# Performance work log

Hardware: AMD Instinct MI355X
Metric: run time of the kernel (lower is better)

The kernel has to match this reference:

```python
import jax, jax.numpy as jnp
import numpy as np
from jax import lax

DN = ('NCHW', 'OIHW', 'NCHW')

def _conv(x, k, stride):
    return lax.conv_general_dilated(x, k, (stride, stride), 'VALID', dimension_numbers=DN)

def setup_inputs() -> dict:
    key = jax.random.key(0)
    ks = jax.random.split(key, 20)
    B, E, A, D = 2048, 8, 6, 64 * 7 * 7  # batch, rm_states, actions, flat conv dim (3136)
    s = 0.05
    inp = {
        'state': jax.random.normal(ks[0], (B, 84, 84, 3), jnp.float32),
        'rm_state': jax.random.randint(ks[1], (B,), 0, E, jnp.int64),
        # conv encoder params
        'k1': jax.random.normal(ks[2], (32, 3, 8, 8), jnp.float32) * s,
        'c1': jnp.zeros((32,), jnp.float32),
        'k2': jax.random.normal(ks[3], (64, 32, 4, 4), jnp.float32) * s,
        'c2': jnp.zeros((64,), jnp.float32),
        'k3': jax.random.normal(ks[4], (64, 64, 3, 3), jnp.float32) * s,
        'c3': jnp.zeros((64,), jnp.float32),
        # stacked per-rm-state expert MLP params (E experts)
        'W1': jax.random.normal(ks[5], (E, D, 64), jnp.float32) * s,
        'B1': jnp.zeros((E, 64), jnp.float32),
        'W2': jax.random.normal(ks[6], (E, 64, 64), jnp.float32) * s,
        'B2': jnp.zeros((E, 64), jnp.float32),
        'W3': jax.random.normal(ks[7], (E, 64, 64), jnp.float32) * s,
        'B3': jnp.zeros((E, 64), jnp.float32),
        'W4': jax.random.normal(ks[8], (E, 64, 64), jnp.float32) * s,
        'B4': jnp.zeros((E, 64), jnp.float32),
        'W5': jax.random.normal(ks[9], (E, 64, 64), jnp.float32) * s,
        'B5': jnp.zeros((E, 64), jnp.float32),
        'W6': jax.random.normal(ks[10], (E, 64, A), jnp.float32) * s,
        'B6': jnp.zeros((E, A), jnp.float32),
    }
    return inp

def reference(state, rm_state, k1, c1, k2, c2, k3, c3,
              W1, B1, W2, B2, W3, B3, W4, B4, W5, B5, W6, B6):
    # NHWC -> NCHW (matches torch's view-based channel-first rearrangement intent)
    x = jnp.transpose(state, (0, 3, 1, 2))
    x = jax.nn.relu(_conv(x, k1, 4) + c1[None, :, None, None])
    x = jax.nn.relu(_conv(x, k2, 2) + c2[None, :, None, None])
    x = jax.nn.relu(_conv(x, k3, 1) + c3[None, :, None, None])
    B = x.shape[0]
    flat = x.reshape(B, -1)                              # [B, 3136]
    # batched expert MLPs: compute all experts, then gather per-sample expert output
    h = jax.nn.relu(jnp.einsum('bd,edh->ebh', flat, W1) + B1[:, None, :])  # [E,B,64]
    for W, Bb in ((W2, B2), (W3, B3), (W4, B4), (W5, B5)):
        h = jax.nn.relu(jnp.einsum('ebh,ehk->ebk', h, W) + Bb[:, None, :])
    out = jnp.einsum('ebh,eha->eba', h, W6) + B6[:, None, :]               # [E,B,A]
    return out[rm_state, jnp.arange(B)]                  # [B, A]
```

## Files before the change

kernel.cpp:

```cpp
#include <hip/hip_runtime.h>

#define BATCH 2048

typedef unsigned short u16;
typedef __attribute__((ext_vector_type(8))) short bf16x8;
typedef __attribute__((ext_vector_type(4))) float f32x4;

static __device__ __forceinline__ float b2f(u16 h) {
  union { unsigned u; float f; } x; x.u = ((unsigned)h) << 16; return x.f;
}
static __device__ __forceinline__ u16 f2b(float f) {
  union { float f; unsigned u; } x; x.f = f;
  return (u16)((x.u + 0x7fffu + ((x.u >> 16) & 1u)) >> 16);
}
static __device__ __forceinline__ void split2(float v, u16& h, u16& l) {
  h = f2b(v); l = f2b(v - b2f(h));
}
static __device__ __forceinline__ bf16x8 ld8u(const u16* p, int idx) {
  union { bf16x8 v; ushort4 u[2]; } x;
  x.u[0] = *(const ushort4*)(p + idx);
  x.u[1] = *(const ushort4*)(p + idx + 4);
  return x.v;
}

__global__ void wsplit_kernel(const float* __restrict__ k1,
                              const float* __restrict__ k2,
                              const float* __restrict__ k3,
                              u16* __restrict__ W1d, u16* __restrict__ W2d,
                              u16* __restrict__ W3d)
{
  int id = blockIdx.x * 256 + threadIdx.x;
  float v; u16 *dh, *dl;
  if (id < 8192) {
    int ky = id >> 10, oc = (id >> 5) & 31, kk = id & 31;
    if (kk < 24) {
      int kx = kk / 3, c = kk - kx * 3;
      v = k1[oc * 192 + c * 64 + ky * 8 + kx];
    } else v = 0.f;
    dh = W1d + id; dl = W1d + 8192 + id;
  } else if (id < 40960) {
    int i = id - 8192;
    int pos = i >> 11, oc = (i >> 5) & 63, cc = i & 31;
    int ky = pos >> 2, kx = pos & 3;
    v = k2[oc * 512 + cc * 16 + ky * 4 + kx];
    dh = W2d + i; dl = W2d + 32768 + i;
  } else {
    int i = id - 40960;
    int j = i & 31, oc = (i >> 5) & 63, kc = (i >> 11) & 1, pos = i >> 12;
    int ky = pos / 3, kx = pos - ky * 3;
    v = k3[oc * 576 + (kc * 32 + j) * 9 + ky * 3 + kx];
    dh = W3d + i; dl = W3d + 36864 + i;
  }
  u16 h, l; split2(v, h, l); *dh = h; *dl = l;
}

__global__ __launch_bounds__(256) void conv_fused_kernel(
    const float* __restrict__ state, const u16* __restrict__ W1d,
    const u16* __restrict__ W2d, const u16* __restrict__ W3d,
    const float* __restrict__ c1, const float* __restrict__ c2,
    const float* __restrict__ c3, float* __restrict__ a3)
{
  __shared__ __align__(16) u16 A1h[14400], A1l[14400];
  __shared__ __align__(16) u16 SHa[5832], SHb[5832];

  const int b = blockIdx.x, t = threadIdx.x;
  const int lane = t & 63, w = t >> 6, q = lane >> 4, n = lane & 15;

  for (int i = t; i < 792; i += 256) { SHa[5040 + i] = 0; SHb[5040 + i] = 0; }

  const bool two = (w < 2);
  const int nPT = two ? 2 : 1, nOT = two ? 2 : 1;
  int ptv[2], otv[2];
  ptv[0] = two ? 2 * w     : 4;
  ptv[1] = two ? 2 * w + 1 : 4;
  otv[0] = two ? 0 : (w - 2);
  otv[1] = 1;

  int aoff1[2];
  #pragma unroll
  for (int i = 0; i < 2; ++i) {
    int px = ptv[i] * 16 + n; if (px > 79) px = 79;
    int py = (px * 205) >> 12, pxx = px - py * 20;
    aoff1[i] = (py * 4) * 252 + pxx * 12 + q * 8;
  }
  float c1v[2];
  #pragma unroll
  for (int j = 0; j < 2; ++j) c1v[j] = c1[otv[j] * 16 + n];

  for (int by = 0; by < 5; ++by) {
    __syncthreads();
    const float4* sp = (const float4*)(state + (size_t)b * 21168 + by * 4032);
    #pragma unroll
    for (int pass = 0; pass < 5; ++pass) {
      int i = t + pass * 256;
      if (i < 1260) {
        float4 v = sp[i];
        u16 h0, l0, h1, l1, h2, l2, h3, l3;
        split2(v.x, h0, l0); split2(v.y, h1, l1);
        split2(v.z, h2, l2); split2(v.w, h3, l3);
        ushort4 hh; hh.x = h0; hh.y = h1; hh.z = h2; hh.w = h3;
        ushort4 ll; ll.x = l0; ll.y = l1; ll.z = l2; ll.w = l3;
        *(ushort4*)&SHa[i * 4] = hh;
        *(ushort4*)&SHb[i * 4] = ll;
      }
    }
    __syncthreads();

    f32x4 acc[2][2] = {};
    for (int ky = 0; ky < 8; ++ky) {
      bf16x8 bh[2], bo[2];
      #pragma unroll
      for (int j = 0; j < 2; ++j) if (j < nOT) {
        int ob = (ky * 32 + otv[j] * 16 + n) * 32 + q * 8;
        bh[j] = *(const bf16x8*)(W1d + ob);
        bo[j] = *(const bf16x8*)(W1d + 8192 + ob);
      }
      #pragma unroll
      for (int i = 0; i < 2; ++i) if (i < nPT) {
        bf16x8 ah = ld8u(SHa, aoff1[i] + ky * 252);
        bf16x8 al = ld8u(SHb, aoff1[i] + ky * 252);
        #pragma unroll
        for (int j = 0; j < 2; ++j) if (j < nOT) {
          acc[i][j] = __builtin_amdgcn_mfma_f32_16x16x32_bf16(ah, bh[j], acc[i][j], 0, 0, 0);
          acc[i][j] = __builtin_amdgcn_mfma_f32_16x16x32_bf16(ah, bo[j], acc[i][j], 0, 0, 0);
          acc[i][j] = __builtin_amdgcn_mfma_f32_16x16x32_bf16(al, bh[j], acc[i][j], 0, 0, 0);
        }
      }
    }
    #pragma unroll
    for (int i = 0; i < 2; ++i) if (i < nPT)
      #pragma unroll
      for (int j = 0; j < 2; ++j) if (j < nOT) {
        int oc = otv[j] * 16 + n;
        #pragma unroll
        for (int r = 0; r < 4; ++r) {
          int px = by * 80 + ptv[i] * 16 + q * 4 + r;
          float v = fmaxf(acc[i][j][r] + c1v[j], 0.f);
          u16 h, l; split2(v, h, l);
          A1h[px * 36 + oc] = h; A1l[px * 36 + oc] = l;
        }
      }
  }
  __syncthreads();

  {
    const int p20 = (w >> 1) * 3, o20 = (w & 1) * 2;
    int aoff2[3];
    #pragma unroll
    for (int i = 0; i < 3; ++i) {
      int px = (p20 + i) * 16 + n; if (px > 80) px = 80;
      int py = (px * 7282) >> 16, pxx = px - py * 9;
      aoff2[i] = 2 * (py * 20 + pxx) * 36 + q * 8;
    }
    float c2v[2];
    #pragma unroll
    for (int j = 0; j < 2; ++j) c2v[j] = c2[(o20 + j) * 16 + n];

    f32x4 acc2[3][2] = {};
    for (int pos = 0; pos < 16; ++pos) {
      const int o = ((pos >> 2) * 20 + (pos & 3)) * 36;
      bf16x8 bh[2], bo[2];
      #pragma unroll
      for (int j = 0; j < 2; ++j) {
        int ob = pos * 2048 + ((o20 + j) * 16 + n) * 32 + q * 8;
        bh[j] = *(const bf16x8*)(W2d + ob);
        bo[j] = *(const bf16x8*)(W2d + 32768 + ob);
      }
      #pragma unroll
      for (int i = 0; i < 3; ++i) {
        bf16x8 ah = ld8u(A1h, aoff2[i] + o);
        bf16x8 al = ld8u(A1l, aoff2[i] + o);
        #pragma unroll
        for (int j = 0; j < 2; ++j) {
          acc2[i][j] = __builtin_amdgcn_mfma_f32_16x16x32_bf16(ah, bh[j], acc2[i][j], 0, 0, 0);
          acc2[i][j] = __builtin_amdgcn_mfma_f32_16x16x32_bf16(ah, bo[j], acc2[i][j], 0, 0, 0);
          acc2[i][j] = __builtin_amdgcn_mfma_f32_16x16x32_bf16(al, bh[j], acc2[i][j], 0, 0, 0);
        }
      }
    }
    #pragma unroll
    for (int i = 0; i < 3; ++i)
      #pragma unroll
      for (int j = 0; j < 2; ++j) {
        int oc = (o20 + j) * 16 + n;
        #pragma unroll
        for (int r = 0; r < 4; ++r) {
          int px = (p20 + i) * 16 + q * 4 + r;
          if (px < 81) {
            float v = fmaxf(acc2[i][j][r] + c2v[j], 0.f);
            u16 h, l; split2(v, h, l);
            SHa[px * 72 + oc] = h; SHb[px * 72 + oc] = l;
          }
        }
      }
  }
  __syncthreads();

  {
    const int p30 = (w >> 1) * 2, o30 = (w & 1) * 2;
    int aoff3[2];
    #pragma unroll
    for (int i = 0; i < 2; ++i) {
      int px = (p30 + i) * 16 + n; if (px > 48) px = 48;
      int py = (px * 74) >> 9, pxx = px - py * 7;
      aoff3[i] = (py * 9 + pxx) * 72 + q * 8;
    }
    float c3v[2];
    #pragma unroll
    for (int j = 0; j < 2; ++j) c3v[j] = c3[(o30 + j) * 16 + n];

    f32x4 acc3[2][2] = {};
    for (int pos = 0; pos < 9; ++pos) {
      int ky = pos / 3, kx = pos - ky * 3;
      const int o = (ky * 9 + kx) * 72;
      #pragma unroll
      for (int kc = 0; kc < 2; ++kc) {
        bf16x8 bh[2], bo[2];
        #pragma unroll
        for (int j = 0; j < 2; ++j) {
          int ob = (pos * 2 + kc) * 2048 + ((o30 + j) * 16 + n) * 32 + q * 8;
          bh[j] = *(const bf16x8*)(W3d + ob);
          bo[j] = *(const bf16x8*)(W3d + 36864 + ob);
        }
        #pragma unroll
        for (int i = 0; i < 2; ++i) {
          bf16x8 ah = *(const bf16x8*)&SHa[aoff3[i] + o + kc * 32];
          bf16x8 al = *(const bf16x8*)&SHb[aoff3[i] + o + kc * 32];
          #pragma unroll
          for (int j = 0; j < 2; ++j) {
            acc3[i][j] = __builtin_amdgcn_mfma_f32_16x16x32_bf16(ah, bh[j], acc3[i][j], 0, 0, 0);
            acc3[i][j] = __builtin_amdgcn_mfma_f32_16x16x32_bf16(ah, bo[j], acc3[i][j], 0, 0, 0);
            acc3[i][j] = __builtin_amdgcn_mfma_f32_16x16x32_bf16(al, bh[j], acc3[i][j], 0, 0, 0);
          }
        }
      }
    }
    float* op = a3 + (size_t)b * 3136;
    #pragma unroll
    for (int i = 0; i < 2; ++i)
      #pragma unroll
      for (int j = 0; j < 2; ++j) {
        int oc = (o30 + j) * 16 + n;
        #pragma unroll
        for (int r = 0; r < 4; ++r) {
          int px = (p30 + i) * 16 + q * 4 + r;
          if (px < 49) op[oc * 49 + px] = fmaxf(acc3[i][j][r] + c3v[j], 0.f);
        }
      }
  }
}

__global__ void group_kernel(const void* __restrict__ rmv,
                             int* __restrict__ counts, int* __restrict__ idxb)
{
  __shared__ int isI32;
  const int t = threadIdx.x;
  if (t == 0) isI32 = 0;
  if (t < 8) counts[t] = 0;
  __syncthreads();
  unsigned long long v = ((const unsigned long long*)rmv)[t];
  if (v >= 8ull) isI32 = 1;
  __syncthreads();
  const int i32 = isI32;
  for (int b = t; b < BATCH; b += 1024) {
    int e = i32 ? ((const int*)rmv)[b] : (int)((const long long*)rmv)[b];
    int pos = atomicAdd(&counts[e], 1);
    idxb[e * BATCH + pos] = b;
  }
}

__global__ __launch_bounds__(256) void gemm1_grp_kernel(
    const float* __restrict__ a3, const int* __restrict__ counts,
    const int* __restrict__ idxb, const float* __restrict__ W1,
    float* __restrict__ H1)
{
  __shared__ __align__(16) float At[32 * 68];
  __shared__ __align__(16) float Bw[32 * 64];
  __shared__ int s_id[64];
  const int e  = blockIdx.x >> 5;
  const int tl = blockIdx.x & 31;
  const int ks = blockIdx.y;
  const int cnt = counts[e];
  const int n0 = tl * 64;
  if (n0 >= cnt) return;
  const int m = min(64, cnt - n0);
  const int t = threadIdx.x;
  if (t < 64) s_id[t] = idxb[e * BATCH + n0 + min(t, m - 1)];
  __syncthreads();

  const int tx = t & 15, ty = t >> 4;
  const int c0 = tx * 4, r0 = ty * 4;
  const float* W1e = W1 + (size_t)e * 3136 * 64;
  float acc[4][4] = {};
  const int kbase = ks * 448;

  for (int k0 = kbase; k0 < kbase + 448; k0 += 32) {
    __syncthreads();
    {
      int i = t;
      #pragma unroll
      for (int pass = 0; pass < 2; ++pass, i += 256) {
        int r = i >> 3, k4 = (i & 7) * 4;
        float4 v = *(const float4*)(a3 + (size_t)s_id[r] * 3136 + k0 + k4);
        At[(k4 + 0) * 68 + r] = v.x; At[(k4 + 1) * 68 + r] = v.y;
        At[(k4 + 2) * 68 + r] = v.z; At[(k4 + 3) * 68 + r] = v.w;
      }
      int i2 = t;
      #pragma unroll
      for (int pass = 0; pass < 2; ++pass, i2 += 256) {
        int kk = i2 >> 4, h4 = (i2 & 15) * 4;
        *(float4*)&Bw[kk * 64 + h4] = *(const float4*)&W1e[(size_t)(k0 + kk) * 64 + h4];
      }
    }
    __syncthreads();
    #pragma unroll
    for (int kk = 0; kk < 32; ++kk) {
      float4 a = *(const float4*)&At[kk * 68 + r0];
      float4 bb = *(const float4*)&Bw[kk * 64 + c0];
      float av[4] = {a.x, a.y, a.z, a.w}, bv[4] = {bb.x, bb.y, bb.z, bb.w};
      #pragma unroll
      for (int ii = 0; ii < 4; ++ii)
        #pragma unroll
        for (int j = 0; j < 4; ++j)
          acc[ii][j] += av[ii] * bv[j];
    }
  }

  #pragma unroll
  for (int ii = 0; ii < 4; ++ii) {
    if (r0 + ii < m) {
      int s = s_id[r0 + ii];
      #pragma unroll
      for (int j = 0; j < 4; ++j)
        atomicAdd(&H1[(size_t)s * 64 + c0 + j], acc[ii][j]);
    }
  }
}

__global__ __launch_bounds__(256) void tail_grp_kernel(
    const float* __restrict__ H1, const int* __restrict__ counts,
    const int* __restrict__ idxb, const float* __restrict__ B1,
    const float* __restrict__ W2, const float* __restrict__ B2,
    const float* __restrict__ W3, const float* __restrict__ B3,
    const float* __restrict__ W4, const float* __restrict__ B4,
    const float* __restrict__ W5, const float* __restrict__ B5,
    const float* __restrict__ W6, const float* __restrict__ B6,
    float* __restrict__ out)
{
  __shared__ __align__(16) float Wl[4096];
  __shared__ float bl[64];
  __shared__ float W6l[384];
  __shared__ float B6l[8];
  __shared__ __align__(16) float Ht0[64 * 68];
  __shared__ __align__(16) float Ht1[64 * 68];
  __shared__ int s_id[64];

  const int e  = blockIdx.x >> 5;
  const int tl = blockIdx.x & 31;
  const int cnt = counts[e];
  const int n0 = tl * 64;
  if (n0 >= cnt) return;
  const int m = min(64, cnt - n0);
  const int t = threadIdx.x;
  if (t < 64) s_id[t] = idxb[e * BATCH + n0 + min(t, m - 1)];
  for (int i = t; i < 384; i += 256) W6l[i] = W6[e * 384 + i];
  if (t < 6)   B6l[t] = B6[e * 6 + t];
  __syncthreads();

  #pragma unroll
  for (int p = 0; p < 16; ++p) {
    int i = t + p * 256;
    int c = i & 63, r = i >> 6;
    Ht0[c * 68 + r] = fmaxf(H1[(size_t)s_id[r] * 64 + c] + B1[e * 64 + c], 0.f);
  }

  const int tx = t & 15, ty = t >> 4;
  const int c0 = tx * 4, r0 = ty * 4;
  const float* Ws[4] = {W2, W3, W4, W5};
  const float* Bs[4] = {B2, B3, B4, B5};
  float* Hc = Ht0; float* Hn = Ht1;

  for (int L = 0; L < 4; ++L) {
    __syncthreads();
    const float* We = Ws[L] + (size_t)e * 4096;
    for (int i = t; i < 1024; i += 256)
      *(float4*)&Wl[i * 4] = *(const float4*)&We[i * 4];
    if (t < 64) bl[t] = Bs[L][e * 64 + t];
    __syncthreads();

    float acc[4][4] = {};
    #pragma unroll 4
    for (int kk = 0; kk < 64; ++kk) {
      float4 a = *(const float4*)&Hc[kk * 68 + r0];
      float4 bb = *(const float4*)&Wl[kk * 64 + c0];
      float av[4] = {a.x, a.y, a.z, a.w}, bv[4] = {bb.x, bb.y, bb.z, bb.w};
      #pragma unroll
      for (int ii = 0; ii < 4; ++ii)
        #pragma unroll
        for (int j = 0; j < 4; ++j)
          acc[ii][j] += av[ii] * bv[j];
    }
    __syncthreads();
    #pragma unroll
    for (int j = 0; j < 4; ++j) {
      float bias = bl[c0 + j];
      #pragma unroll
      for (int ii = 0; ii < 4; ++ii)
        Hn[(c0 + j) * 68 + r0 + ii] = fmaxf(acc[ii][j] + bias, 0.f);
    }
    float* tmp = Hc; Hc = Hn; Hn = tmp;
  }
  __syncthreads();

  const int r = t & 63, aa = t >> 6;
  float s0v = 0.f, s1v = 0.f;
  for (int k = 0; k < 64; ++k) {
    float h = Hc[k * 68 + r];
    s0v += h * W6l[k * 6 + aa];
    s1v += h * W6l[k * 6 + ((aa < 2) ? aa + 4 : aa)];
  }
  if (r < m) {
    int s = s_id[r];
    out[s * 6 + aa] = s0v + B6l[aa];
    if (aa < 2) out[s * 6 + aa + 4] = s1v + B6l[aa + 4];
  }
}

extern "C" void kernel_launch(void* const* d_in, const int* in_sizes, int n_in,
                              void* d_out, int out_size, void* d_ws, size_t ws_size,
                              hipStream_t stream) {
  const float* state = (const float*)d_in[0];
  const void*  rm    = d_in[1];
  const float* k1 = (const float*)d_in[2];
  const float* c1 = (const float*)d_in[3];
  const float* k2 = (const float*)d_in[4];
  const float* c2 = (const float*)d_in[5];
  const float* k3 = (const float*)d_in[6];
  const float* c3 = (const float*)d_in[7];
  const float* W1 = (const float*)d_in[8];
  const float* B1 = (const float*)d_in[9];
  const float* W2 = (const float*)d_in[10];
  const float* B2 = (const float*)d_in[11];
  const float* W3 = (const float*)d_in[12];
  const float* B3 = (const float*)d_in[13];
  const float* W4 = (const float*)d_in[14];
  const float* B4 = (const float*)d_in[15];
  const float* W5 = (const float*)d_in[16];
  const float* B5 = (const float*)d_in[17];
  const float* W6 = (const float*)d_in[18];
  const float* B6 = (const float*)d_in[19];

  char* ws = (char*)d_ws;
  float* a3   = (float*)(ws);
  float* H1   = (float*)(ws + 25690112);
  int* counts = (int*)  (ws + 26214400);
  int* idxb   = (int*)  (ws + 26214432);
  u16* W1d    = (u16*)  (ws + 26280064);
  u16* W2d    = (u16*)  (ws + 26312832);
  u16* W3d    = (u16*)  (ws + 26443904);

  wsplit_kernel<<<304, 256, 0, stream>>>(k1, k2, k3, W1d, W2d, W3d);
  hipMemsetAsync(H1, 0, BATCH * 64 * sizeof(float), stream);
  group_kernel<<<1, 1024, 0, stream>>>(rm, counts, idxb);

  conv_fused_kernel<<<2048, 256, 0, stream>>>(state, W1d, W2d, W3d,
                                              c1, c2, c3, a3);

  gemm1_grp_kernel<<<dim3(256, 7), 256, 0, stream>>>(a3, counts, idxb, W1, H1);
  tail_grp_kernel<<<256, 256, 0, stream>>>(H1, counts, idxb, B1,
                                           W2, B2, W3, B3, W4, B4, W5, B5,
                                           W6, B6, (float*)d_out);
}
```

Before: 539.8 us.

## Use 512-thread blocks in fused conv and prefetch weight fragments

Each conv block now has 8 waves instead of 4. Every wave owns a single output-channel tile and fewer pixel tiles in all three conv stages, and the state load uses 3 passes instead of 5. Weight fragments for the next kernel position are loaded one step ahead, a register double buffer meant to hide global load latency behind the MFMAs. Launch bounds change to (512,4) to request higher occupancy, which could cap registers and cause spills. Shared memory per block stays about the same.

```diff
diff --git a/kernel.cpp b/kernel.cpp
--- a/kernel.cpp
+++ b/kernel.cpp
@@ -54,7 +54,7 @@
   u16 h, l; split2(v, h, l); *dh = h; *dl = l;
 }
 
-__global__ __launch_bounds__(256) void conv_fused_kernel(
+__global__ __launch_bounds__(512, 4) void conv_fused_kernel(
     const float* __restrict__ state, const u16* __restrict__ W1d,
     const u16* __restrict__ W2d, const u16* __restrict__ W3d,
     const float* __restrict__ c1, const float* __restrict__ c2,
@@ -66,33 +66,32 @@
   const int b = blockIdx.x, t = threadIdx.x;
   const int lane = t & 63, w = t >> 6, q = lane >> 4, n = lane & 15;
 
-  for (int i = t; i < 792; i += 256) { SHa[5040 + i] = 0; SHb[5040 + i] = 0; }
-
-  const bool two = (w < 2);
-  const int nPT = two ? 2 : 1, nOT = two ? 2 : 1;
-  int ptv[2], otv[2];
-  ptv[0] = two ? 2 * w     : 4;
-  ptv[1] = two ? 2 * w + 1 : 4;
-  otv[0] = two ? 0 : (w - 2);
-  otv[1] = 1;
+  for (int i = t; i < 792; i += 512) { SHa[5040 + i] = 0; SHb[5040 + i] = 0; }
+
+  const int nT1 = (w < 2) ? 2 : 1;
+  int pt1[2], ot1[2];
+  if (w < 2) { pt1[0] = 0; ot1[0] = w; pt1[1] = 4; ot1[1] = w; }
+  else       { pt1[0] = 1 + ((w - 2) >> 1); ot1[0] = (w - 2) & 1;
+               pt1[1] = pt1[0]; ot1[1] = ot1[0]; }
 
   int aoff1[2];
   #pragma unroll
   for (int i = 0; i < 2; ++i) {
-    int px = ptv[i] * 16 + n; if (px > 79) px = 79;
+    int px = pt1[i] * 16 + n;
     int py = (px * 205) >> 12, pxx = px - py * 20;
     aoff1[i] = (py * 4) * 252 + pxx * 12 + q * 8;
   }
   float c1v[2];
   #pragma unroll
-  for (int j = 0; j < 2; ++j) c1v[j] = c1[otv[j] * 16 + n];
+  for (int j = 0; j < 2; ++j) c1v[j] = c1[ot1[j] * 16 + n];
+  const int ob1 = (ot1[0] * 16 + n) * 32 + q * 8;
 
   for (int by = 0; by < 5; ++by) {
     __syncthreads();
     const float4* sp = (const float4*)(state + (size_t)b * 21168 + by * 4032);
     #pragma unroll
-    for (int pass = 0; pass < 5; ++pass) {
-      int i = t + pass * 256;
+    for (int pass = 0; pass < 3; ++pass) {
+      int i = t + pass * 512;
       if (i < 1260) {
         float4 v = sp[i];
         u16 h0, l0, h1, l1, h2, l2, h3, l3;
@@ -106,147 +105,125 @@
     }
     __syncthreads();
 
-    f32x4 acc[2][2] = {};
+    f32x4 acc1[2] = {};
+    bf16x8 bhc = *(const bf16x8*)(W1d + ob1);
+    bf16x8 boc = *(const bf16x8*)(W1d + 8192 + ob1);
     for (int ky = 0; ky < 8; ++ky) {
-      bf16x8 bh[2], bo[2];
-      #pragma unroll
-      for (int j = 0; j < 2; ++j) if (j < nOT) {
-        int ob = (ky * 32 + otv[j] * 16 + n) * 32 + q * 8;
-        bh[j] = *(const bf16x8*)(W1d + ob);
-        bo[j] = *(const bf16x8*)(W1d + 8192 + ob);
-      }
-      #pragma unroll
-      for (int i = 0; i < 2; ++i) if (i < nPT) {
+      const int kyn = (ky < 7) ? ky + 1 : 7;
+      bf16x8 bhn = *(const bf16x8*)(W1d + kyn * 1024 + ob1);
+      bf16x8 bon = *(const bf16x8*)(W1d + 8192 + kyn * 1024 + ob1);
+      #pragma unroll
+      for (int i = 0; i < 2; ++i) if (i < nT1) {
         bf16x8 ah = ld8u(SHa, aoff1[i] + ky * 252);
         bf16x8 al = ld8u(SHb, aoff1[i] + ky * 252);
-        #pragma unroll
-        for (int j = 0; j < 2; ++j) if (j < nOT) {
-          acc[i][j] = __builtin_amdgcn_mfma_f32_16x16x32_bf16(ah, bh[j], acc[i][j], 0, 0, 0);
-          acc[i][j] = __builtin_amdgcn_mfma_f32_16x16x32_bf16(ah, bo[j], acc[i][j], 0, 0, 0);
-          acc[i][j] = __builtin_amdgcn_mfma_f32_16x16x32_bf16(al, bh[j], acc[i][j], 0, 0, 0);
-        }
-      }
-    }
-    #pragma unroll
-    for (int i = 0; i < 2; ++i) if (i < nPT)
-      #pragma unroll
-      for (int j = 0; j < 2; ++j) if (j < nOT) {
-        int oc = otv[j] * 16 + n;
-        #pragma unroll
-        for (int r = 0; r < 4; ++r) {
-          int px = by * 80 + ptv[i] * 16 + q * 4 + r;
-          float v = fmaxf(acc[i][j][r] + c1v[j], 0.f);
-          u16 h, l; split2(v, h, l);
-          A1h[px * 36 + oc] = h; A1l[px * 36 + oc] = l;
-        }
-      }
+        acc1[i] = __builtin_amdgcn_mfma_f32_16x16x32_bf16(ah, bhc, acc1[i], 0, 0, 0);
+        acc1[i] = __builtin_amdgcn_mfma_f32_16x16x32_bf16(ah, boc, acc1[i], 0, 0, 0);
+        acc1[i] = __builtin_amdgcn_mfma_f32_16x16x32_bf16(al, bhc, acc1[i], 0, 0, 0);
+      }
+      bhc = bhn; boc = bon;
+    }
+    #pragma unroll
+    for (int i = 0; i < 2; ++i) if (i < nT1) {
+      int oc = ot1[i] * 16 + n;
+      #pragma unroll
+      for (int r = 0; r < 4; ++r) {
+        int px = by * 80 + pt1[i] * 16 + q * 4 + r;
+        float v = fmaxf(acc1[i][r] + c1v[i], 0.f);
+        u16 h, l; split2(v, h, l);
+        A1h[px * 36 + oc] = h; A1l[px * 36 + oc] = l;
+      }
+    }
   }
   __syncthreads();
 
   {
-    const int p20 = (w >> 1) * 3, o20 = (w & 1) * 2;
+    const int ot2 = w & 3, pg2 = (w >> 2) * 3;
     int aoff2[3];
     #pragma unroll
     for (int i = 0; i < 3; ++i) {
-      int px = (p20 + i) * 16 + n; if (px > 80) px = 80;
+      int px = (pg2 + i) * 16 + n; if (px > 80) px = 80;
       int py = (px * 7282) >> 16, pxx = px - py * 9;
       aoff2[i] = 2 * (py * 20 + pxx) * 36 + q * 8;
     }
-    float c2v[2];
-    #pragma unroll
-    for (int j = 0; j < 2; ++j) c2v[j] = c2[(o20 + j) * 16 + n];
-
-    f32x4 acc2[3][2] = {};
+    const float c2v = c2[ot2 * 16 + n];
+    const int ob2 = (ot2 * 16 + n) * 32 + q * 8;
+
+    f32x4 acc2[3] = {};
+    bf16x8 bhc = *(const bf16x8*)(W2d + ob2);
+    bf16x8 boc = *(const bf16x8*)(W2d + 32768 + ob2);
     for (int pos = 0; pos < 16; ++pos) {
+      const int posn = (pos < 15) ? pos + 1 : 15;
+      bf16x8 bhn = *(const bf16x8*)(W2d + posn * 2048 + ob2);
+      bf16x8 bon = *(const bf16x8*)(W2d + 32768 + posn * 2048 + ob2);
       const int o = ((pos >> 2) * 20 + (pos & 3)) * 36;
-      bf16x8 bh[2], bo[2];
-      #pragma unroll
-      for (int j = 0; j < 2; ++j) {
-        int ob = pos * 2048 + ((o20 + j) * 16 + n) * 32 + q * 8;
-        bh[j] = *(const bf16x8*)(W2d + ob);
-        bo[j] = *(const bf16x8*)(W2d + 32768 + ob);
-      }
       #pragma unroll
       for (int i = 0; i < 3; ++i) {
         bf16x8 ah = ld8u(A1h, aoff2[i] + o);
         bf16x8 al = ld8u(A1l, aoff2[i] + o);
-        #pragma unroll
-        for (int j = 0; j < 2; ++j) {
-          acc2[i][j] = __builtin_amdgcn_mfma_f32_16x16x32_bf16(ah, bh[j], acc2[i][j], 0, 0, 0);
-          acc2[i][j] = __builtin_amdgcn_mfma_f32_16x16x32_bf16(ah, bo[j], acc2[i][j], 0, 0, 0);
-          acc2[i][j] = __builtin_amdgcn_mfma_f32_16x16x32_bf16(al, bh[j], acc2[i][j], 0, 0, 0);
+        acc2[i] = __builtin_amdgcn_mfma_f32_16x16x32_bf16(ah, bhc, acc2[i], 0, 0, 0);
+        acc2[i] = __builtin_amdgcn_mfma_f32_16x16x32_bf16(ah, boc, acc2[i], 0, 0, 0);
+        acc2[i] = __builtin_amdgcn_mfma_f32_16x16x32_bf16(al, bhc, acc2[i], 0, 0, 0);
+      }
+      bhc = bhn; boc = bon;
+    }
+    #pragma unroll
+    for (int i = 0; i < 3; ++i) {
+      int oc = ot2 * 16 + n;
+      #pragma unroll
+      for (int r = 0; r < 4; ++r) {
+        int px = (pg2 + i) * 16 + q * 4 + r;
+        if (px < 81) {
+          float v = fmaxf(acc2[i][r] + c2v, 0.f);
+          u16 h, l; split2(v, h, l);
+          SHa[px * 72 + oc] = h; SHb[px * 72 + oc] = l;
         }
       }
     }
-    #pragma unroll
-    for (int i = 0; i < 3; ++i)
-      #pragma unroll
-      for (int j = 0; j < 2; ++j) {
-        int oc = (o20 + j) * 16 + n;
-        #pragma unroll
-        for (int r = 0; r < 4; ++r) {
-          int px = (p20 + i) * 16 + q * 4 + r;
-          if (px < 81) {
-            float v = fmaxf(acc2[i][j][r] + c2v[j], 0.f);
-            u16 h, l; split2(v, h, l);
-            SHa[px * 72 + oc] = h; SHb[px * 72 + oc] = l;
-          }
-        }
-      }
   }
   __syncthreads();
 
   {
-    const int p30 = (w >> 1) * 2, o30 = (w & 1) * 2;
+    const int ot3 = w & 3, pg3 = (w >> 2) * 2;
     int aoff3[2];
     #pragma unroll
     for (int i = 0; i < 2; ++i) {
-      int px = (p30 + i) * 16 + n; if (px > 48) px = 48;
+      int px = (pg3 + i) * 16 + n; if (px > 48) px = 48;
       int py = (px * 74) >> 9, pxx = px - py * 7;
       aoff3[i] = (py * 9 + pxx) * 72 + q * 8;
     }
-    float c3v[2];
-    #pragma unroll
-    for (int j = 0; j < 2; ++j) c3v[j] = c3[(o30 + j) * 16 + n];
-
-    f32x4 acc3[2][2] = {};
-    for (int pos = 0; pos < 9; ++pos) {
-      int ky = pos / 3, kx = pos - ky * 3;
-      const int o = (ky * 9 + kx) * 72;
-      #pragma unroll
-      for (int kc = 0; kc < 2; ++kc) {
-        bf16x8 bh[2], bo[2];
-        #pragma unroll
-        for (int j = 0; j < 2; ++j) {
-          int ob = (pos * 2 + kc) * 2048 + ((o30 + j) * 16 + n) * 32 + q * 8;
-          bh[j] = *(const bf16x8*)(W3d + ob);
-          bo[j] = *(const bf16x8*)(W3d + 36864 + ob);
-        }
-        #pragma unroll
-        for (int i = 0; i < 2; ++i) {
-          bf16x8 ah = *(const bf16x8*)&SHa[aoff3[i] + o + kc * 32];
-          bf16x8 al = *(const bf16x8*)&SHb[aoff3[i] + o + kc * 32];
-          #pragma unroll
-          for (int j = 0; j < 2; ++j) {
-            acc3[i][j] = __builtin_amdgcn_mfma_f32_16x16x32_bf16(ah, bh[j], acc3[i][j], 0, 0, 0);
-            acc3[i][j] = __builtin_amdgcn_mfma_f32_16x16x32_bf16(ah, bo[j], acc3[i][j], 0, 0, 0);
-            acc3[i][j] = __builtin_amdgcn_mfma_f32_16x16x32_bf16(al, bh[j], acc3[i][j], 0, 0, 0);
-          }
-        }
-      }
+    const float c3v = c3[ot3 * 16 + n];
+    const int ob3 = (ot3 * 16 + n) * 32 + q * 8;
+
+    f32x4 acc3[2] = {};
+    bf16x8 bhc = *(const bf16x8*)(W3d + ob3);
+    bf16x8 boc = *(const bf16x8*)(W3d + 36864 + ob3);
+    for (int pk = 0; pk < 18; ++pk) {
+      const int pkn = (pk < 17) ? pk + 1 : 17;
+      bf16x8 bhn = *(const bf16x8*)(W3d + pkn * 2048 + ob3);
+      bf16x8 bon = *(const bf16x8*)(W3d + 36864 + pkn * 2048 + ob3);
+      const int pos = pk >> 1, kc = pk & 1;
+      const int ky = pos / 3, kx = pos - ky * 3;
+      const int o = (ky * 9 + kx) * 72 + kc * 32;
+      #pragma unroll
+      for (int i = 0; i < 2; ++i) {
+        bf16x8 ah = *(const bf16x8*)&SHa[aoff3[i] + o];
+        bf16x8 al = *(const bf16x8*)&SHb[aoff3[i] + o];
+        acc3[i] = __builtin_amdgcn_mfma_f32_16x16x32_bf16(ah, bhc, acc3[i], 0, 0, 0);
+        acc3[i] = __builtin_amdgcn_mfma_f32_16x16x32_bf16(ah, boc, acc3[i], 0, 0, 0);
+        acc3[i] = __builtin_amdgcn_mfma_f32_16x16x32_bf16(al, bhc, acc3[i], 0, 0, 0);
+      }
+      bhc = bhn; boc = bon;
     }
     float* op = a3 + (size_t)b * 3136;
     #pragma unroll
-    for (int i = 0; i < 2; ++i)
-      #pragma unroll
-      for (int j = 0; j < 2; ++j) {
-        int oc = (o30 + j) * 16 + n;
-        #pragma unroll
-        for (int r = 0; r < 4; ++r) {
-          int px = (p30 + i) * 16 + q * 4 + r;
-          if (px < 49) op[oc * 49 + px] = fmaxf(acc3[i][j][r] + c3v[j], 0.f);
-        }
-      }
+    for (int i = 0; i < 2; ++i) {
+      int oc = ot3 * 16 + n;
+      #pragma unroll
+      for (int r = 0; r < 4; ++r) {
+        int px = (pg3 + i) * 16 + q * 4 + r;
+        if (px < 49) op[oc * 49 + px] = fmaxf(acc3[i][r] + c3v, 0.f);
+      }
+    }
   }
 }
 
@@ -463,7 +440,7 @@
   hipMemsetAsync(H1, 0, BATCH * 64 * sizeof(float), stream);
   group_kernel<<<1, 1024, 0, stream>>>(rm, counts, idxb);
 
-  conv_fused_kernel<<<2048, 256, 0, stream>>>(state, W1d, W2d, W3d,
+  conv_fused_kernel<<<2048, 512, 0, stream>>>(state, W1d, W2d, W3d,
                                               c1, c2, c3, a3);
 
   gemm1_grp_kernel<<<dim3(256, 7), 256, 0, stream>>>(a3, counts, idxb, W1, H1);
```

After: 489.1 us. -9.4%, faster.
